# Performance work log

Hardware: AMD Instinct MI355X
Metric: run time of the kernel (lower is better)

## Reference

```python
import jax, jax.numpy as jnp
import numpy as np

K = 9  # kernel_size (kNN neighbors, includes self since loop=True)


def _knn_edges(x_f, batch, k):
    # x_f: [N, C]. Full pairwise squared distances, masked across batch groups.
    N = x_f.shape[0]
    sq = jnp.sum(x_f * x_f, axis=1)
    d2 = sq[:, None] - 2.0 * (x_f @ x_f.T) + sq[None, :]          # [N, N]
    same = batch[:, None] == batch[None, :]
    d2 = jnp.where(same, d2, jnp.inf)
    neg_d, idx = jax.lax.top_k(-d2, k)                             # k nearest per query row
    valid = jnp.isfinite(neg_d)                                    # guard tiny groups (<k nodes)
    src = idx.reshape(-1)                                          # neighbor -> source
    tgt = jnp.repeat(jnp.arange(N), k)                             # query    -> target
    return src, tgt, valid.reshape(-1)


def _cheb_conv(x_f, src, tgt, valid, W0, W1, bias):
    # ChebConv, K=2, normalization='sym', lambda_max=2.0:
    #   out = x @ W0 + (L_hat x) @ W1 + b,  L_hat = -D^{-1/2} A D^{-1/2} (diag 0)
    N = x_f.shape[0]
    w = jnp.where(valid & (src != tgt), 1.0, 0.0)                  # remove_self_loops
    deg = jax.ops.segment_sum(w, src, num_segments=N)
    dis = jnp.where(deg > 0, jax.lax.rsqrt(jnp.maximum(deg, 1e-30)), 0.0)
    norm = -dis[src] * w * dis[tgt]                                # off-diag of scaled Laplacian
    Tx1 = jax.ops.segment_sum(norm[:, None] * x_f[src], tgt, num_segments=N)
    return x_f @ W0 + Tx1 @ W1 + bias


def setup_inputs() -> dict:
    key = jax.random.key(0)
    k1, k2, k3, k4 = jax.random.split(key, 4)
    B, C, H, W = 8, 192, 32, 32
    Cout = 192
    return {
        "x": jax.random.normal(k1, (B, C, H, W), dtype=jnp.float32),
        "W0": jax.random.normal(k2, (C, Cout), dtype=jnp.float32) * (1.0 / np.sqrt(C)),
        "W1": jax.random.normal(k3, (C, Cout), dtype=jnp.float32) * (1.0 / np.sqrt(C)),
        "bias": jax.random.normal(k4, (Cout,), dtype=jnp.float32) * 0.01,
    }


def reference(x, W0, W1, bias):
    B, C, H, W = x.shape
    N = B * H * W
    x_f = jnp.transpose(x, (0, 2, 3, 1)).reshape(N, C)             # flat_nodes: [B*H*W, C]
    # torch.linspace(0, B, steps=N, dtype=int64) -> truncated float linspace
    batch = jnp.linspace(0.0, float(B), N).astype(jnp.int32)
    src, tgt, valid = _knn_edges(x_f, batch, K)
    return _cheb_conv(x_f, src, tgt, valid, W0, W1, bias)
```

## Files before the change

kernel.cpp:

```cpp
#include <hip/hip_runtime.h>
#include <math.h>

#define NN 8192
#define CF 192
#define KNN 9
#define NSPL 8

typedef __bf16 v8bf __attribute__((ext_vector_type(8)));
typedef float f32x16 __attribute__((ext_vector_type(16)));
typedef float f32x4 __attribute__((ext_vector_type(4)));

__device__ __forceinline__ int group_start(int g) {
    int s = (8191 * g + 7) >> 3;
    return s > 8192 ? 8192 : s;
}

__device__ __forceinline__ float disf(int d) {
    return d > 0 ? 1.0f / sqrtf((float)d) : 0.0f;
}

__device__ __forceinline__ unsigned short f2bf(float f) {
    unsigned u = __float_as_uint(f);
    unsigned r = (u + 0x7FFFu + ((u >> 16) & 1u)) >> 16;
    return (unsigned short)r;
}
__device__ __forceinline__ float bf2f(unsigned short h) {
    return __uint_as_float(((unsigned)h) << 16);
}

__global__ __launch_bounds__(256) void transpose_kernel(
    const float* __restrict__ x, unsigned short* __restrict__ xh,
    unsigned short* __restrict__ xl, float* __restrict__ sq,
    int* __restrict__ deg)
{
    __shared__ float tile[32][65];
    int b = blockIdx.x, ht = blockIdx.y;
    int hw0 = ht * 64;
    int tid = threadIdx.x;
    if (tid < 64) deg[(b * 16 + ht) * 64 + tid] = 0;

    float sacc[8];
#pragma unroll
    for (int p = 0; p < 8; ++p) sacc[p] = 0.0f;

    for (int ct = 0; ct < 6; ++ct) {
        int c0 = ct * 32;
        __syncthreads();
#pragma unroll
        for (int p = 0; p < 8; ++p) {
            int c  = p * 4 + (tid >> 6);
            int hw = tid & 63;
            tile[c][hw] = x[(size_t)b * 196608 + (size_t)(c0 + c) * 1024 + hw0 + hw];
        }
        __syncthreads();
#pragma unroll
        for (int p = 0; p < 8; ++p) {
            int hw = p * 8 + (tid >> 5);
            int cc = tid & 31;
            float v = tile[cc][hw];
            size_t o = (size_t)(b * 1024 + hw0 + hw) * CF + c0 + cc;
            unsigned short h = f2bf(v);
            xh[o] = h;
            xl[o] = f2bf(v - bf2f(h));
            sacc[p] = fmaf(v, v, sacc[p]);
        }
    }
#pragma unroll
    for (int p = 0; p < 8; ++p) {
        float s = sacc[p];
#pragma unroll
        for (int off = 16; off > 0; off >>= 1) s += __shfl_xor(s, off, 32);
        if ((tid & 31) == 0)
            sq[(size_t)(b * 1024 + hw0 + p * 8 + (tid >> 5))] = s;
    }
}

__global__ __launch_bounds__(256, 2) void knn_kernel(
    const unsigned short* __restrict__ xh, const unsigned short* __restrict__ xl,
    const float* __restrict__ sq,
    float* __restrict__ pk_d, int* __restrict__ pk_i)
{
    int bid = blockIdx.x;
    int g = bid >> 7;
    int rem = bid & 127;
    int qb = rem >> 3;
    int split = rem & 7;
    int gs = group_start(g);
    int gsize = group_start(g + 1) - gs;
    int q0 = qb * 64;
    int nq = gsize - q0; if (nq > 64) nq = 64;
    if (nq <= 0) return;
    int c0 = split * 128;
    int ncc = gsize - c0; if (ncc > 128) ncc = 128;

    int tid = threadIdx.x;

    float td[KNN]; int ti[KNN];
#pragma unroll
    for (int j = 0; j < KNN; ++j) { td[j] = __builtin_inff(); ti[j] = -1; }

    if (ncc <= 0) {
        if (tid < nq) {
            int q = gs + q0 + tid;
            size_t base = ((size_t)q * NSPL + split) * KNN;
#pragma unroll
            for (int j = 0; j < KNN; ++j) { pk_d[base + j] = td[j]; pk_i[base + j] = ti[j]; }
        }
        return;
    }

    __shared__ __align__(16) char smem[28192];
    unsigned short (*Ah)[24] = (unsigned short(*)[24])smem;
    unsigned short (*Al)[24] = (unsigned short(*)[24])(smem + 3072);
    unsigned short (*Bh)[24] = (unsigned short(*)[24])(smem + 6144);
    unsigned short (*Bl)[24] = (unsigned short(*)[24])(smem + 12288);
    float (*ld)[KNN][65] = (float(*)[KNN][65])smem;
    int   (*li)[KNN][65] = (int(*)[KNN][65])(smem + 9360);
    float (*Ds)[37] = (float(*)[37])(smem + 18720);
    __shared__ float sqc_s[128];
    __shared__ float sqq_s[64];

    int lane = tid & 63, w = tid >> 6;
    int arow = (w & 1) * 32 + (lane & 31);
    int k8 = (lane >> 5) * 8;
    int brow0 = (w >> 1) * 64 + (lane & 31);

    if (tid < 64) {
        int qo = q0 + tid; if (qo > gsize - 1) qo = gsize - 1;
        sqq_s[tid] = sq[gs + qo];
    }
    if (tid < 128) {
        sqc_s[tid] = (tid < ncc) ? sq[gs + c0 + tid] : __builtin_inff();
    }

    int a_hl = tid >> 7, a_r = (tid >> 1) & 63, a_half = tid & 1;
    int a_qo = q0 + a_r; if (a_qo > gsize - 1) a_qo = gsize - 1;
    const unsigned short* a_src = (a_hl ? xl : xh)
        + (size_t)(gs + a_qo) * CF + a_half * 8;
    unsigned short* a_dst = (a_hl ? (unsigned short*)Al : (unsigned short*)Ah)
        + a_r * 24 + a_half * 8;

    f32x16 acc[2];
#pragma unroll
    for (int t = 0; t < 2; ++t)
#pragma unroll
        for (int r = 0; r < 16; ++r) acc[t][r] = 0.0f;

    for (int kb = 0; kb < 12; ++kb) {
        __syncthreads();
        *(uint4*)a_dst = *(const uint4*)(a_src + kb * 16);
#pragma unroll
        for (int p = 0; p < 2; ++p) {
            int t = tid + 256 * p;
            int hl = t >> 8, r = (t >> 1) & 127, half = t & 1;
            int co = c0 + r; if (co > gsize - 1) co = gsize - 1;
            const unsigned short* src = (hl ? xl : xh)
                + (size_t)(gs + co) * CF + kb * 16 + half * 8;
            unsigned short* dst = (hl ? (unsigned short*)Bl : (unsigned short*)Bh)
                + r * 24 + half * 8;
            *(uint4*)dst = *(const uint4*)src;
        }
        __syncthreads();
        v8bf a_hi = *(const v8bf*)&Ah[arow][k8];
        v8bf a_lo = *(const v8bf*)&Al[arow][k8];
#pragma unroll
        for (int t = 0; t < 2; ++t) {
            v8bf b_hi = *(const v8bf*)&Bh[brow0 + t * 32][k8];
            v8bf b_lo = *(const v8bf*)&Bl[brow0 + t * 32][k8];
            acc[t] = __builtin_amdgcn_mfma_f32_32x32x16_bf16(a_hi, b_hi, acc[t], 0, 0, 0);
            acc[t] = __builtin_amdgcn_mfma_f32_32x32x16_bf16(a_lo, b_hi, acc[t], 0, 0, 0);
            acc[t] = __builtin_amdgcn_mfma_f32_32x32x16_bf16(a_hi, b_lo, acc[t], 0, 0, 0);
        }
    }

#pragma unroll
    for (int qt = 0; qt < 4; ++qt) {
        __syncthreads();
        if ((w >> 1) == (qt >> 1)) {
#pragma unroll
            for (int r = 0; r < 16; ++r) {
                int row = (w & 1) * 32 + (r & 3) + 8 * (r >> 2) + 4 * (lane >> 5);
                Ds[row][lane & 31] = acc[qt & 1][r];
            }
        }
        __syncthreads();
        {
            int q = tid & 63, ch = tid >> 6;
            float sqq = sqq_s[q];
            float pd[KNN]; int pi[KNN];
#pragma unroll
            for (int j = 0; j < KNN; ++j) { pd[j] = __builtin_inff(); pi[j] = -1; }
#pragma unroll
            for (int j8 = 0; j8 < 8; ++j8) {
                int c = ch * 8 + j8;
                float d = (sqq - 2.0f * Ds[q][c]) + sqc_s[qt * 32 + c];
                if (d < pd[KNN - 1]) {
                    pd[KNN - 1] = d; pi[KNN - 1] = gs + c0 + qt * 32 + c;
#pragma unroll
                    for (int j = KNN - 1; j > 0; --j) {
                        if (pd[j] < pd[j - 1]) {
                            float tf = pd[j]; pd[j] = pd[j - 1]; pd[j - 1] = tf;
                            int tn = pi[j]; pi[j] = pi[j - 1]; pi[j - 1] = tn;
                        }
                    }
                }
            }
#pragma unroll
            for (int j = 0; j < KNN; ++j) { ld[ch][j][q] = pd[j]; li[ch][j][q] = pi[j]; }
        }
        __syncthreads();
        if (tid < 64) {
            for (int ch = 0; ch < 4; ++ch) {
#pragma unroll
                for (int j0 = 0; j0 < KNN; ++j0) {
                    float d = ld[ch][j0][tid];
                    if (!(d < td[KNN - 1])) break;
                    int id = li[ch][j0][tid];
                    td[KNN - 1] = d; ti[KNN - 1] = id;
#pragma unroll
                    for (int j = KNN - 1; j > 0; --j) {
                        if (td[j] < td[j - 1]) {
                            float tf = td[j]; td[j] = td[j - 1]; td[j - 1] = tf;
                            int tn = ti[j]; ti[j] = ti[j - 1]; ti[j - 1] = tn;
                        }
                    }
                }
            }
        }
    }

    if (tid < nq) {
        int q = gs + q0 + tid;
        size_t base = ((size_t)q * NSPL + split) * KNN;
#pragma unroll
        for (int j = 0; j < KNN; ++j) { pk_d[base + j] = td[j]; pk_i[base + j] = ti[j]; }
    }
}

__global__ __launch_bounds__(64) void merge_kernel(
    const float* __restrict__ pk_d, const int* __restrict__ pk_i,
    int* __restrict__ edges, int* __restrict__ deg,
    const float* __restrict__ W0, const float* __restrict__ W1,
    unsigned short* __restrict__ wt)
{
    __shared__ float wtile[32][33];
    int tid = threadIdx.x;
    if (blockIdx.x >= 128) {
        int wid = blockIdx.x - 128;
        int mat = wid / 36, rem2 = wid % 36;
        int k0 = (rem2 / 6) * 32, n0 = (rem2 % 6) * 32;
        const float* W = mat ? W1 : W0;
#pragma unroll
        for (int p = 0; p < 4; ++p) {
            int idx = p * 64 + tid;
            int k = idx >> 3, n4 = (idx & 7) * 4;
            *(float4*)&wtile[k][n4] =
                *(const float4*)(W + (size_t)(k0 + k) * CF + n0 + n4);
        }
        __syncthreads();
#pragma unroll
        for (int p = 0; p < 4; ++p) {
            int idx = p * 64 + tid;
            int n = idx >> 3, k4 = (idx & 7) * 4;
            ushort4 h;
            h.x = f2bf(wtile[k4 + 0][n]); h.y = f2bf(wtile[k4 + 1][n]);
            h.z = f2bf(wtile[k4 + 2][n]); h.w = f2bf(wtile[k4 + 3][n]);
            *(ushort4*)(wt + (size_t)mat * 36864 + (size_t)(n0 + n) * CF + k0 + k4) = h;
        }
        return;
    }
    int q = blockIdx.x * 64 + tid;
    float td[KNN]; int ti[KNN];
#pragma unroll
    for (int j = 0; j < KNN; ++j) { td[j] = __builtin_inff(); ti[j] = -1; }
    for (int s = 0; s < NSPL; ++s) {
        size_t base = ((size_t)q * NSPL + s) * KNN;
#pragma unroll
        for (int j0 = 0; j0 < KNN; ++j0) {
            float d = pk_d[base + j0];
            if (!(d < td[KNN - 1])) break;
            int id = pk_i[base + j0];
            td[KNN - 1] = d; ti[KNN - 1] = id;
#pragma unroll
            for (int j = KNN - 1; j > 0; --j) {
                if (td[j] < td[j - 1]) {
                    float tf = td[j]; td[j] = td[j - 1]; td[j - 1] = tf;
                    int tn = ti[j]; ti[j] = ti[j - 1]; ti[j - 1] = tn;
                }
            }
        }
    }
#pragma unroll
    for (int j = 0; j < KNN; ++j) {
        int id = ti[j];
        edges[q * KNN + j] = id;
        if (id >= 0 && id != q) atomicAdd(&deg[id], 1);
    }
}

__global__ __launch_bounds__(256, 2) void out_kernel(
    const unsigned short* __restrict__ xh, const unsigned short* __restrict__ wt,
    const int* __restrict__ edges, const int* __restrict__ deg,
    const float* __restrict__ bias, float* __restrict__ out)
{
    __shared__ unsigned short A0s[16][200];
    __shared__ unsigned short A1s[16][200];
    __shared__ unsigned short Wts[2][CF][32];
    __shared__ float coef_s[16][KNN];
    __shared__ int   nb_s[16][KNN];

    int r0 = blockIdx.x * 16;
    int tid = threadIdx.x;

    for (int t = tid; t < 384; t += 256) {
        int i = t / 24, c8 = (t % 24) * 8;
        *(uint4*)&A0s[i][c8] = *(const uint4*)(xh + (size_t)(r0 + i) * CF + c8);
    }
    if (tid < 16 * KNN) {
        int i = tid / KNN, j = tid % KNN;
        int q = r0 + i;
        int id = edges[q * KNN + j];
        float cf = 0.0f; int s = q;
        if (id >= 0 && id != q) { cf = -disf(deg[id]) * disf(deg[q]); s = id; }
        coef_s[i][j] = cf; nb_s[i][j] = s;
    }
    __syncthreads();
    for (int e = tid; e < 16 * CF / 2; e += 256) {
        int i = e / 96, c2 = (e % 96) * 2;
        float a0 = 0.0f, a1 = 0.0f;
#pragma unroll
        for (int t = 0; t < KNN; ++t) {
            const unsigned short* row = xh + (size_t)nb_s[i][t] * CF + c2;
            float cf = coef_s[i][t];
            a0 = fmaf(cf, bf2f(row[0]), a0);
            a1 = fmaf(cf, bf2f(row[1]), a1);
        }
        ushort2 h; h.x = f2bf(a0); h.y = f2bf(a1);
        *(ushort2*)&A1s[i][c2] = h;
    }

    int lane = tid & 63, w = tid >> 6;
    int m = lane & 15;
    int kq = (lane >> 4) * 8;
    f32x4 acc[3];
#pragma unroll
    for (int t = 0; t < 3; ++t)
#pragma unroll
        for (int r = 0; r < 4; ++r) acc[t][r] = 0.0f;

    for (int kt = 0; kt < 6; ++kt) {
        __syncthreads();
#pragma unroll
        for (int p = 0; p < 6; ++p) {
            int f = p * 256 + tid;
            int mat = f / 768, n = (f % 768) / 4, k16 = (f % 4) * 8;
            *(uint4*)&Wts[mat][n][k16] =
                *(const uint4*)(wt + (size_t)mat * 36864 + (size_t)n * CF + kt * 32 + k16);
        }
        __syncthreads();
        v8bf a0 = *(const v8bf*)&A0s[m][kt * 32 + kq];
        v8bf a1 = *(const v8bf*)&A1s[m][kt * 32 + kq];
#pragma unroll
        for (int t3 = 0; t3 < 3; ++t3) {
            int n0 = w * 48 + t3 * 16;
            v8bf w0 = *(const v8bf*)&Wts[0][n0 + m][kq];
            v8bf w1 = *(const v8bf*)&Wts[1][n0 + m][kq];
            acc[t3] = __builtin_amdgcn_mfma_f32_16x16x32_bf16(a0, w0, acc[t3], 0, 0, 0);
            acc[t3] = __builtin_amdgcn_mfma_f32_16x16x32_bf16(a1, w1, acc[t3], 0, 0, 0);
        }
    }

    int col = lane & 15, rb = (lane >> 4) * 4;
#pragma unroll
    for (int t3 = 0; t3 < 3; ++t3) {
        int n0 = w * 48 + t3 * 16;
        float bv = bias[n0 + col];
#pragma unroll
        for (int r = 0; r < 4; ++r)
            out[(size_t)(r0 + rb + r) * CF + n0 + col] = acc[t3][r] + bv;
    }
}

extern "C" void kernel_launch(void* const* d_in, const int* in_sizes, int n_in,
                              void* d_out, int out_size, void* d_ws, size_t ws_size,
                              hipStream_t stream)
{
    const float* x    = (const float*)d_in[0];
    const float* W0   = (const float*)d_in[1];
    const float* W1   = (const float*)d_in[2];
    const float* bias = (const float*)d_in[3];
    float* out = (float*)d_out;

    char* ws = (char*)d_ws;
    unsigned short* xh = (unsigned short*)ws; ws += (size_t)NN * CF * 2;
    unsigned short* xl = (unsigned short*)ws; ws += (size_t)NN * CF * 2;
    float* sq    = (float*)ws;  ws += (size_t)NN * 4;
    int*   deg   = (int*)ws;    ws += (size_t)NN * 4;
    int*   edges = (int*)ws;    ws += (size_t)NN * KNN * 4;

    unsigned short* wt = xl;

    float* pk_d = out;
    int*   pk_i = (int*)(out + (size_t)NN * NSPL * KNN);

    hipLaunchKernelGGL(transpose_kernel, dim3(8, 16), dim3(256), 0, stream,
                       x, xh, xl, sq, deg);
    hipLaunchKernelGGL(knn_kernel, dim3(1152), dim3(256), 0, stream,
                       xh, xl, sq, pk_d, pk_i);
    hipLaunchKernelGGL(merge_kernel, dim3(200), dim3(64), 0, stream,
                       pk_d, pk_i, edges, deg, W0, W1, wt);
    hipLaunchKernelGGL(out_kernel, dim3(512), dim3(256), 0, stream,
                       xh, wt, edges, deg, bias, out);
}
```

Measured before the change: 144.1 us.

## Split transpose over channel tiles and halve out_kernel row tile

The transpose kernel now launches one block per (batch, channel tile, spatial tile) instead of looping over six channel tiles, giving six times more blocks. Squared norms are accumulated with atomicAdd into sq, which is zeroed together with deg by a memset. The output kernel handles 8 rows per block instead of 16, doubling the grid to fill more CUs. In exchange, half of each 16-row MFMA tile is wasted work, the W tiles are reloaded twice as often, and atomics make the float sums order-dependent.

```diff
diff --git a/kernel.cpp b/kernel.cpp
--- a/kernel.cpp
+++ b/kernel.cpp
@@ -30,48 +30,32 @@
 
 __global__ __launch_bounds__(256) void transpose_kernel(
     const float* __restrict__ x, unsigned short* __restrict__ xh,
-    unsigned short* __restrict__ xl, float* __restrict__ sq,
-    int* __restrict__ deg)
+    unsigned short* __restrict__ xl, float* __restrict__ sq)
 {
     __shared__ float tile[32][65];
-    int b = blockIdx.x, ht = blockIdx.y;
-    int hw0 = ht * 64;
+    int b = blockIdx.x, ct = blockIdx.y, ht = blockIdx.z;
+    int c0 = ct * 32, hw0 = ht * 64;
     int tid = threadIdx.x;
-    if (tid < 64) deg[(b * 16 + ht) * 64 + tid] = 0;
-
-    float sacc[8];
-#pragma unroll
-    for (int p = 0; p < 8; ++p) sacc[p] = 0.0f;
-
-    for (int ct = 0; ct < 6; ++ct) {
-        int c0 = ct * 32;
-        __syncthreads();
-#pragma unroll
-        for (int p = 0; p < 8; ++p) {
-            int c  = p * 4 + (tid >> 6);
-            int hw = tid & 63;
-            tile[c][hw] = x[(size_t)b * 196608 + (size_t)(c0 + c) * 1024 + hw0 + hw];
-        }
-        __syncthreads();
-#pragma unroll
-        for (int p = 0; p < 8; ++p) {
-            int hw = p * 8 + (tid >> 5);
-            int cc = tid & 31;
-            float v = tile[cc][hw];
-            size_t o = (size_t)(b * 1024 + hw0 + hw) * CF + c0 + cc;
-            unsigned short h = f2bf(v);
-            xh[o] = h;
-            xl[o] = f2bf(v - bf2f(h));
-            sacc[p] = fmaf(v, v, sacc[p]);
-        }
-    }
 #pragma unroll
     for (int p = 0; p < 8; ++p) {
-        float s = sacc[p];
-#pragma unroll
-        for (int off = 16; off > 0; off >>= 1) s += __shfl_xor(s, off, 32);
-        if ((tid & 31) == 0)
-            sq[(size_t)(b * 1024 + hw0 + p * 8 + (tid >> 5))] = s;
+        int c  = p * 4 + (tid >> 6);
+        int hw = tid & 63;
+        tile[c][hw] = x[(size_t)b * 196608 + (size_t)(c0 + c) * 1024 + hw0 + hw];
+    }
+    __syncthreads();
+#pragma unroll
+    for (int p = 0; p < 8; ++p) {
+        int hw = p * 8 + (tid >> 5);
+        int cc = tid & 31;
+        float v = tile[cc][hw];
+        size_t o = (size_t)(b * 1024 + hw0 + hw) * CF + c0 + cc;
+        unsigned short h = f2bf(v);
+        xh[o] = h;
+        xl[o] = f2bf(v - bf2f(h));
+        float s = v * v;
+#pragma unroll
+        for (int off = 16; off > 0; off >>= 1) s += __shfl_xor(s, off, 64);
+        if (cc == 0) atomicAdd(&sq[b * 1024 + hw0 + hw], s);
     }
 }
 
@@ -303,20 +287,20 @@
     const int* __restrict__ edges, const int* __restrict__ deg,
     const float* __restrict__ bias, float* __restrict__ out)
 {
-    __shared__ unsigned short A0s[16][200];
-    __shared__ unsigned short A1s[16][200];
+    __shared__ unsigned short A0s[8][200];
+    __shared__ unsigned short A1s[8][200];
     __shared__ unsigned short Wts[2][CF][32];
-    __shared__ float coef_s[16][KNN];
-    __shared__ int   nb_s[16][KNN];
-
-    int r0 = blockIdx.x * 16;
+    __shared__ float coef_s[8][KNN];
+    __shared__ int   nb_s[8][KNN];
+
+    int r0 = blockIdx.x * 8;
     int tid = threadIdx.x;
 
-    for (int t = tid; t < 384; t += 256) {
-        int i = t / 24, c8 = (t % 24) * 8;
+    if (tid < 192) {
+        int i = tid / 24, c8 = (tid % 24) * 8;
         *(uint4*)&A0s[i][c8] = *(const uint4*)(xh + (size_t)(r0 + i) * CF + c8);
     }
-    if (tid < 16 * KNN) {
+    if (tid < 8 * KNN) {
         int i = tid / KNN, j = tid % KNN;
         int q = r0 + i;
         int id = edges[q * KNN + j];
@@ -325,7 +309,9 @@
         coef_s[i][j] = cf; nb_s[i][j] = s;
     }
     __syncthreads();
-    for (int e = tid; e < 16 * CF / 2; e += 256) {
+#pragma unroll
+    for (int p = 0; p < 3; ++p) {
+        int e = tid + 256 * p;
         int i = e / 96, c2 = (e % 96) * 2;
         float a0 = 0.0f, a1 = 0.0f;
 #pragma unroll
@@ -340,7 +326,8 @@
     }
 
     int lane = tid & 63, w = tid >> 6;
-    int m = lane & 15;
+    int am = lane & 7;
+    int n16 = lane & 15;
     int kq = (lane >> 4) * 8;
     f32x4 acc[3];
 #pragma unroll
@@ -358,26 +345,28 @@
                 *(const uint4*)(wt + (size_t)mat * 36864 + (size_t)n * CF + kt * 32 + k16);
         }
         __syncthreads();
-        v8bf a0 = *(const v8bf*)&A0s[m][kt * 32 + kq];
-        v8bf a1 = *(const v8bf*)&A1s[m][kt * 32 + kq];
+        v8bf a0 = *(const v8bf*)&A0s[am][kt * 32 + kq];
+        v8bf a1 = *(const v8bf*)&A1s[am][kt * 32 + kq];
 #pragma unroll
         for (int t3 = 0; t3 < 3; ++t3) {
             int n0 = w * 48 + t3 * 16;
-            v8bf w0 = *(const v8bf*)&Wts[0][n0 + m][kq];
-            v8bf w1 = *(const v8bf*)&Wts[1][n0 + m][kq];
+            v8bf w0 = *(const v8bf*)&Wts[0][n0 + n16][kq];
+            v8bf w1 = *(const v8bf*)&Wts[1][n0 + n16][kq];
             acc[t3] = __builtin_amdgcn_mfma_f32_16x16x32_bf16(a0, w0, acc[t3], 0, 0, 0);
             acc[t3] = __builtin_amdgcn_mfma_f32_16x16x32_bf16(a1, w1, acc[t3], 0, 0, 0);
         }
     }
 
-    int col = lane & 15, rb = (lane >> 4) * 4;
-#pragma unroll
-    for (int t3 = 0; t3 < 3; ++t3) {
-        int n0 = w * 48 + t3 * 16;
-        float bv = bias[n0 + col];
-#pragma unroll
-        for (int r = 0; r < 4; ++r)
-            out[(size_t)(r0 + rb + r) * CF + n0 + col] = acc[t3][r] + bv;
+    if (lane < 32) {
+        int col = lane & 15, rb = (lane >> 4) * 4;
+#pragma unroll
+        for (int t3 = 0; t3 < 3; ++t3) {
+            int n0 = w * 48 + t3 * 16;
+            float bv = bias[n0 + col];
+#pragma unroll
+            for (int r = 0; r < 4; ++r)
+                out[(size_t)(r0 + rb + r) * CF + n0 + col] = acc[t3][r] + bv;
+        }
     }
 }
 
@@ -403,12 +392,13 @@
     float* pk_d = out;
     int*   pk_i = (int*)(out + (size_t)NN * NSPL * KNN);
 
-    hipLaunchKernelGGL(transpose_kernel, dim3(8, 16), dim3(256), 0, stream,
-                       x, xh, xl, sq, deg);
+    hipMemsetAsync(sq, 0, (size_t)NN * 8, stream);
+    hipLaunchKernelGGL(transpose_kernel, dim3(8, 6, 16), dim3(256), 0, stream,
+                       x, xh, xl, sq);
     hipLaunchKernelGGL(knn_kernel, dim3(1152), dim3(256), 0, stream,
                        xh, xl, sq, pk_d, pk_i);
     hipLaunchKernelGGL(merge_kernel, dim3(200), dim3(64), 0, stream,
                        pk_d, pk_i, edges, deg, W0, W1, wt);
-    hipLaunchKernelGGL(out_kernel, dim3(512), dim3(256), 0, stream,
+    hipLaunchKernelGGL(out_kernel, dim3(1024), dim3(256), 0, stream,
                        xh, wt, edges, deg, bias, out);
 }
```

Result: no change. 146.5 us (+1.6%).
